# Kernel tuning notes

Hardware: AMD Instinct MI355X
Metric: run time of the kernel (lower is better)

## Reference

```python
import jax, jax.numpy as jnp
import numpy as np

D_MODEL = 128
DEPTH = 4
LN_EPS = 1e-5


def _ssm(x, Wi, A, Wo):
    # x: [B, L, D]; Wi: [3D, D]; A: [D]; Wo: [D, D]
    z = jnp.einsum('bld,ed->ble', x, Wi)          # [B, L, 3D]
    u, i, o = jnp.split(z, 3, axis=-1)
    iu = jax.nn.sigmoid(i) * jnp.tanh(u)          # gated input, [B, L, D]
    og = jax.nn.sigmoid(o)                        # output gate
    a = jnp.minimum(jnp.exp(A), 0.999)            # decay, [D]

    def step(s, c):
        s = a * s + c
        return s, s

    s0 = jnp.zeros((x.shape[0], x.shape[2]), x.dtype)
    _, S = jax.lax.scan(step, s0, jnp.swapaxes(iu, 0, 1))  # [L, B, D]
    y = og * jnp.swapaxes(S, 0, 1)                # [B, L, D]
    return jnp.einsum('bld,ed->ble', y, Wo)


def _scan_2d(x, Wi, A, Wo):
    # x: [N, D, H, W] -> four directional 1D scans, averaged
    N, D, H, W = x.shape
    xh = jnp.transpose(x, (0, 2, 3, 1))           # [N, H, W, D]
    lr = _ssm(xh.reshape(N * H, W, D), Wi, A, Wo).reshape(N, H, W, D)
    rl = _ssm(jnp.flip(xh, 2).reshape(N * H, W, D), Wi, A, Wo).reshape(N, H, W, D)
    rl = jnp.flip(rl, 2)
    xw = jnp.transpose(x, (0, 3, 2, 1))           # [N, W, H, D]
    ud = _ssm(xw.reshape(N * W, H, D), Wi, A, Wo).reshape(N, W, H, D)
    du = _ssm(jnp.flip(xw, 2).reshape(N * W, H, D), Wi, A, Wo).reshape(N, W, H, D)
    du = jnp.flip(du, 2)
    y = (lr + rl + jnp.transpose(ud, (0, 2, 1, 3)) + jnp.transpose(du, (0, 2, 1, 3))) / 4
    return jnp.transpose(y, (0, 3, 1, 2))         # [N, D, H, W]


def setup_inputs() -> dict:
    key = jax.random.key(0)
    ks = jax.random.split(key, 8)
    D = D_MODEL
    lin = 1.0 / np.sqrt(D)
    tok = jax.random.normal(ks[0], (8, 16, D, 32, 32), jnp.float32)
    s_inp = jax.random.normal(ks[1], (DEPTH, 3 * D, D), jnp.float32) * lin
    s_A = jax.random.normal(ks[2], (DEPTH, D), jnp.float32) * -0.1
    s_out = jax.random.normal(ks[3], (DEPTH, D, D), jnp.float32) * lin
    t_inp = jax.random.normal(ks[4], (DEPTH, 3 * D, D), jnp.float32) * lin
    t_A = jax.random.normal(ks[5], (DEPTH, D), jnp.float32) * -0.1
    t_out = jax.random.normal(ks[6], (DEPTH, D, D), jnp.float32) * lin
    ln_g = jnp.ones((D,), jnp.float32)
    ln_b = jnp.zeros((D,), jnp.float32)
    return {"tok": tok, "s_inp": s_inp, "s_A": s_A, "s_out": s_out,
            "t_inp": t_inp, "t_A": t_A, "t_out": t_out,
            "ln_g": ln_g, "ln_b": ln_b}


def reference(tok, s_inp, s_A, s_out, t_inp, t_A, t_out, ln_g, ln_b):
    B, T, D, h, w = tok.shape
    x = tok
    for l in range(DEPTH):
        xs = x.reshape(B * T, D, h, w)
        xs = _scan_2d(xs, s_inp[l], s_A[l], s_out[l]).reshape(B, T, D, h, w)
        xt = jnp.transpose(xs, (0, 3, 4, 1, 2)).reshape(B * h * w, T, D)
        xt = _ssm(xt, t_inp[l], t_A[l], t_out[l]).reshape(B, h, w, T, D)
        x = x + jnp.transpose(xt, (0, 3, 4, 1, 2))
    xn = jnp.transpose(x, (0, 1, 3, 4, 2))        # [B,T,h,w,D]
    mu = jnp.mean(xn, axis=-1, keepdims=True)
    var = jnp.var(xn, axis=-1, keepdims=True)
    xn = (xn - mu) / jnp.sqrt(var + LN_EPS) * ln_g + ln_b
    return jnp.transpose(xn, (0, 1, 4, 2, 3))     # [B,T,D,h,w]
```

## Files before the change

### kernel.cpp

```cpp
#include <hip/hip_runtime.h>
#include <hip/hip_bf16.h>
#include <math.h>

#define D_MODEL 128
#define HW      1024
#define DEPTH   4
#define NIMG    128
#define B_      8
#define T_      16
#define LN_EPSF 1e-5f

typedef short  s8  __attribute__((ext_vector_type(8)));
typedef ushort us8 __attribute__((ext_vector_type(8)));
typedef ushort us4 __attribute__((ext_vector_type(4)));
typedef float  f4  __attribute__((ext_vector_type(4)));

__device__ __forceinline__ float sig_(float x) { return 1.0f / (1.0f + __expf(-x)); }
__device__ __forceinline__ float tanh_(float x) { return 2.0f * sig_(2.0f * x) - 1.0f; }
__device__ __forceinline__ ushort f2b(float f) {
    __hip_bfloat16 h = __float2bfloat16(f);
    return *reinterpret_cast<ushort*>(&h);
}
__device__ __forceinline__ float b2f(ushort u) {
    __hip_bfloat16 h = *reinterpret_cast<__hip_bfloat16*>(&u);
    return __bfloat162float(h);
}

__global__ __launch_bounds__(256) void wconv_kernel(
    const float* __restrict__ src, ushort* __restrict__ dst, int n)
{
    int i = blockIdx.x * 256 + threadIdx.x;
    if (i < n) dst[i] = f2b(src[i]);
}

__device__ __forceinline__ void gates_from_lds(
    const ushort (*Xs)[136], const ushort* __restrict__ Wi,
    ushort* __restrict__ iu, ushort* __restrict__ og,
    size_t nbase, int q0, int tid)
{
    const int lane = tid & 63;
    const int wv   = tid >> 6;
    const int grp  = lane >> 4;
    const int lrow = lane & 15;
    const int ch0  = wv * 32;

    f4 aU[2][4], aI[2][4], aO[2][4];
    #pragma unroll
    for (int nt = 0; nt < 2; ++nt)
        #pragma unroll
        for (int qt = 0; qt < 4; ++qt) { aU[nt][qt] = (f4)0.f; aI[nt][qt] = (f4)0.f; aO[nt][qt] = (f4)0.f; }

    #pragma unroll
    for (int kk = 0; kk < 4; ++kk) {
        const int kb = kk * 32 + grp * 8;
        s8 xb[4], wu[2], wi[2], wo[2];
        #pragma unroll
        for (int qt = 0; qt < 4; ++qt)
            xb[qt] = *reinterpret_cast<const s8*>(&Xs[qt * 16 + lrow][kb]);
        #pragma unroll
        for (int nt = 0; nt < 2; ++nt) {
            const int e = ch0 + nt * 16 + lrow;
            wu[nt] = *reinterpret_cast<const s8*>(Wi + (size_t)e * D_MODEL + kb);
            wi[nt] = *reinterpret_cast<const s8*>(Wi + (size_t)(e + 128) * D_MODEL + kb);
            wo[nt] = *reinterpret_cast<const s8*>(Wi + (size_t)(e + 256) * D_MODEL + kb);
        }
        #pragma unroll
        for (int nt = 0; nt < 2; ++nt)
            #pragma unroll
            for (int qt = 0; qt < 4; ++qt) {
                aU[nt][qt] = __builtin_amdgcn_mfma_f32_16x16x32_bf16(wu[nt], xb[qt], aU[nt][qt], 0, 0, 0);
                aI[nt][qt] = __builtin_amdgcn_mfma_f32_16x16x32_bf16(wi[nt], xb[qt], aI[nt][qt], 0, 0, 0);
                aO[nt][qt] = __builtin_amdgcn_mfma_f32_16x16x32_bf16(wo[nt], xb[qt], aO[nt][qt], 0, 0, 0);
            }
    }

    #pragma unroll
    for (int nt = 0; nt < 2; ++nt)
        #pragma unroll
        for (int qt = 0; qt < 4; ++qt) {
            const int q = q0 + qt * 16 + lrow;
            const size_t off = nbase + (size_t)q * D_MODEL + ch0 + nt * 16 + grp * 4;
            us4 piu, pog;
            #pragma unroll
            for (int i = 0; i < 4; ++i) {
                piu[i] = f2b(sig_(aI[nt][qt][i]) * tanh_(aU[nt][qt][i]));
                pog[i] = f2b(sig_(aO[nt][qt][i]));
            }
            *reinterpret_cast<us4*>(iu + off) = piu;
            *reinterpret_cast<us4*>(og + off) = pog;
        }
}

__device__ __forceinline__ void stage1_gfrags(
    const ushort* __restrict__ S, const ushort* __restrict__ og,
    float scale, size_t nbase, int q0, int wv, int grp, int lrow, s8 g[4])
{
    const size_t rbase = nbase + (size_t)(q0 + wv * 16 + lrow) * D_MODEL + grp * 8;
    #pragma unroll
    for (int kk = 0; kk < 4; ++kk) {
        const size_t off = rbase + kk * 32;
        us8 sv = *reinterpret_cast<const us8*>(S + off);
        us8 ov = *reinterpret_cast<const us8*>(og + off);
        s8 gg;
        #pragma unroll
        for (int j = 0; j < 8; ++j)
            gg[j] = (short)f2b(b2f(sv[j]) * b2f(ov[j]) * scale);
        g[kk] = gg;
    }
}

__global__ __launch_bounds__(256, 2) void gates_f32_kernel(
    const float* __restrict__ in, const ushort* __restrict__ Wi,
    ushort* __restrict__ iu, ushort* __restrict__ og)
{
    __shared__ ushort Xs[64][136];
    const int n   = blockIdx.x >> 4;
    const int q0  = (blockIdx.x & 15) << 6;
    const int tid = threadIdx.x;
    const size_t nbase = (size_t)n * (D_MODEL * HW);

    {
        const float* inb = in + nbase + q0;
        const int q   = tid & 63;
        const int dh0 = tid >> 6;
        for (int it = 0; it < 4; ++it) {
            const int dh = dh0 + it * 4;
            s8 pk;
            #pragma unroll
            for (int j = 0; j < 8; ++j)
                pk[j] = (short)f2b(inb[(size_t)(dh * 8 + j) * HW + q]);
            *reinterpret_cast<s8*>(&Xs[q][dh * 8]) = pk;
        }
    }
    __syncthreads();
    gates_from_lds(Xs, Wi, iu, og, nbase, q0, tid);
}

__global__ __launch_bounds__(256, 2) void fusedA_kernel(
    const ushort* __restrict__ S, const ushort* __restrict__ og_in,
    const ushort* __restrict__ Wo, const ushort* __restrict__ Wi2,
    ushort* __restrict__ iu, ushort* __restrict__ og, float scale)
{
    __shared__ ushort Xs[64][136];
    const int n   = blockIdx.x >> 4;
    const int q0  = (blockIdx.x & 15) << 6;
    const int tid = threadIdx.x;
    const int lane = tid & 63, wv = tid >> 6, grp = lane >> 4, lrow = lane & 15;
    const size_t nbase = (size_t)n * (D_MODEL * HW);

    s8 g[4];
    stage1_gfrags(S, og_in, scale, nbase, q0, wv, grp, lrow, g);

    f4 C[8];
    #pragma unroll
    for (int et = 0; et < 8; ++et) C[et] = (f4)0.f;
    #pragma unroll
    for (int kk = 0; kk < 4; ++kk) {
        const int kb = kk * 32 + grp * 8;
        #pragma unroll
        for (int et = 0; et < 8; ++et) {
            s8 wf = *reinterpret_cast<const s8*>(Wo + (size_t)(et * 16 + lrow) * D_MODEL + kb);
            C[et] = __builtin_amdgcn_mfma_f32_16x16x32_bf16(g[kk], wf, C[et], 0, 0, 0);
        }
    }

    #pragma unroll
    for (int et = 0; et < 8; ++et)
        #pragma unroll
        for (int i = 0; i < 4; ++i)
            Xs[wv * 16 + grp * 4 + i][et * 16 + lrow] = f2b(C[et][i]);
    __syncthreads();

    gates_from_lds(Xs, Wi2, iu, og, nbase, q0, tid);
}

template <bool GATES, bool LN>
__global__ __launch_bounds__(256, 2) void fusedB_kernel(
    const ushort* __restrict__ S, const ushort* __restrict__ og_in,
    const ushort* __restrict__ Wo, const float* __restrict__ resid,
    float* __restrict__ X, const ushort* __restrict__ Wi2,
    ushort* __restrict__ iu, ushort* __restrict__ og,
    const float* __restrict__ lng, const float* __restrict__ lnb)
{
    __shared__ ushort Xs[64][136];
    const int n   = blockIdx.x >> 4;
    const int q0  = (blockIdx.x & 15) << 6;
    const int tid = threadIdx.x;
    const int lane = tid & 63, wv = tid >> 6, grp = lane >> 4, lrow = lane & 15;
    const size_t nbase = (size_t)n * (D_MODEL * HW);

    s8 g[4];
    stage1_gfrags(S, og_in, 1.0f, nbase, q0, wv, grp, lrow, g);

    f4 C[8];
    #pragma unroll
    for (int et = 0; et < 8; ++et) C[et] = (f4)0.f;
    #pragma unroll
    for (int kk = 0; kk < 4; ++kk) {
        const int kb = kk * 32 + grp * 8;
        #pragma unroll
        for (int et = 0; et < 8; ++et) {
            s8 wf = *reinterpret_cast<const s8*>(Wo + (size_t)(et * 16 + lrow) * D_MODEL + kb);
            C[et] = __builtin_amdgcn_mfma_f32_16x16x32_bf16(g[kk], wf, C[et], 0, 0, 0);
        }
    }

    const int qb = q0 + wv * 16 + grp * 4;

    if constexpr (LN) {
        float sum[4] = {0.f, 0.f, 0.f, 0.f}, sq[4] = {0.f, 0.f, 0.f, 0.f};
        #pragma unroll
        for (int et = 0; et < 8; ++et) {
            const int e = et * 16 + lrow;
            const size_t off = nbase + (size_t)e * HW + qb;
            f4 r = *reinterpret_cast<const f4*>(resid + off);
            #pragma unroll
            for (int i = 0; i < 4; ++i) {
                float v = C[et][i] + r[i];
                C[et][i] = v;
                sum[i] += v; sq[i] += v * v;
            }
        }
        #pragma unroll
        for (int m = 1; m <= 8; m <<= 1)
            #pragma unroll
            for (int i = 0; i < 4; ++i) {
                sum[i] += __shfl_xor(sum[i], m);
                sq[i]  += __shfl_xor(sq[i], m);
            }
        float mean[4], rstd[4];
        #pragma unroll
        for (int i = 0; i < 4; ++i) {
            mean[i] = sum[i] * (1.f / D_MODEL);
            float var = sq[i] * (1.f / D_MODEL) - mean[i] * mean[i];
            rstd[i] = rsqrtf(var + LN_EPSF);
        }
        #pragma unroll
        for (int et = 0; et < 8; ++et) {
            const int e = et * 16 + lrow;
            const float ge = lng[e], be = lnb[e];
            const size_t off = nbase + (size_t)e * HW + qb;
            f4 o;
            #pragma unroll
            for (int i = 0; i < 4; ++i)
                o[i] = (C[et][i] - mean[i]) * rstd[i] * ge + be;
            *reinterpret_cast<f4*>(X + off) = o;
        }
    } else {
        #pragma unroll
        for (int et = 0; et < 8; ++et) {
            const int e = et * 16 + lrow;
            const size_t off = nbase + (size_t)e * HW + qb;
            f4 r = *reinterpret_cast<const f4*>(resid + off);
            f4 v;
            #pragma unroll
            for (int i = 0; i < 4; ++i) v[i] = C[et][i] + r[i];
            *reinterpret_cast<f4*>(X + off) = v;
            if constexpr (GATES) {
                #pragma unroll
                for (int i = 0; i < 4; ++i)
                    Xs[wv * 16 + grp * 4 + i][e] = f2b(v[i]);
            }
        }
        if constexpr (GATES) {
            __syncthreads();
            gates_from_lds(Xs, Wi2, iu, og, nbase, q0, tid);
        }
    }
}

__global__ __launch_bounds__(256) void rowscan_kernel(
    const ushort* __restrict__ iu, ushort* __restrict__ R,
    const float* __restrict__ Av)
{
    const int tid = blockIdx.x * 256 + threadIdx.x;
    const int d = tid & 127;
    const int i = (tid >> 7) & 31;
    const int n = tid >> 12;
    const float a = fminf(__expf(Av[d]), 0.999f);
    const size_t base = (size_t)n * (D_MODEL * HW) + (size_t)(i * 32) * D_MODEL + d;

    float x[32], acc[32];
    #pragma unroll
    for (int j = 0; j < 32; ++j) x[j] = b2f(iu[base + (size_t)j * D_MODEL]);
    float s = 0.f;
    #pragma unroll
    for (int j = 0; j < 32; ++j) { s = fmaf(a, s, x[j]); acc[j] = s; }
    s = 0.f;
    #pragma unroll
    for (int j = 31; j >= 0; --j) { s = fmaf(a, s, x[j]); acc[j] += s; }
    #pragma unroll
    for (int j = 0; j < 32; ++j) R[base + (size_t)j * D_MODEL] = f2b(acc[j]);
}

__global__ __launch_bounds__(256) void colscan_kernel(
    ushort* __restrict__ buf, const ushort* __restrict__ R,
    const float* __restrict__ Av)
{
    const int tid = blockIdx.x * 256 + threadIdx.x;
    const int d = tid & 127;
    const int j = (tid >> 7) & 31;
    const int n = tid >> 12;
    const float a = fminf(__expf(Av[d]), 0.999f);
    const size_t base = (size_t)n * (D_MODEL * HW) + (size_t)j * D_MODEL + d;
    const size_t istr = (size_t)32 * D_MODEL;

    float x[32], t[32];
    #pragma unroll
    for (int i = 0; i < 32; ++i) x[i] = b2f(buf[base + i * istr]);
    float s = 0.f;
    #pragma unroll
    for (int i = 0; i < 32; ++i) { s = fmaf(a, s, x[i]); t[i] = s; }
    s = 0.f;
    #pragma unroll
    for (int i = 31; i >= 0; --i) { s = fmaf(a, s, x[i]); t[i] += s; }
    #pragma unroll
    for (int i = 0; i < 32; ++i)
        buf[base + i * istr] = f2b(t[i] + b2f(R[base + i * istr]));
}

__global__ __launch_bounds__(256) void tscan_kernel(
    ushort* __restrict__ buf, const float* __restrict__ Av)
{
    const int tid = blockIdx.x * 256 + threadIdx.x;
    const int dc = tid & 15;
    const int q  = (tid >> 4) & 1023;
    const int b  = tid >> 14;
    float aa[8], st[8];
    #pragma unroll
    for (int jj = 0; jj < 8; ++jj) {
        aa[jj] = fminf(__expf(Av[dc * 8 + jj]), 0.999f);
        st[jj] = 0.f;
    }
    #pragma unroll
    for (int t = 0; t < T_; ++t) {
        const size_t off = ((size_t)(b * T_ + t) * HW + q) * D_MODEL + dc * 8;
        us8 v = *reinterpret_cast<us8*>(buf + off);
        us8 w;
        #pragma unroll
        for (int jj = 0; jj < 8; ++jj) {
            st[jj] = fmaf(aa[jj], st[jj], b2f(v[jj]));
            w[jj] = f2b(st[jj]);
        }
        *reinterpret_cast<us8*>(buf + off) = w;
    }
}

extern "C" void kernel_launch(void* const* d_in, const int* in_sizes, int n_in,
                              void* d_out, int out_size, void* d_ws, size_t ws_size,
                              hipStream_t stream) {
    const float* tok   = (const float*)d_in[0];
    const float* s_inp = (const float*)d_in[1];
    const float* s_A   = (const float*)d_in[2];
    const float* s_out = (const float*)d_in[3];
    const float* t_inp = (const float*)d_in[4];
    const float* t_A   = (const float*)d_in[5];
    const float* t_out = (const float*)d_in[6];
    const float* ln_g  = (const float*)d_in[7];
    const float* ln_b  = (const float*)d_in[8];

    float*  X    = (float*)d_out;
    ushort* Abuf = (ushort*)d_ws;
    ushort* Bbuf = Abuf + (size_t)16777216;
    ushort* Cbuf = Bbuf + (size_t)16777216;
    ushort* Wbf  = Cbuf + (size_t)16777216;
    ushort* sWiB = Wbf;
    ushort* sWoB = Wbf + 196608;
    ushort* tWiB = Wbf + 262144;
    ushort* tWoB = Wbf + 458752;

    const dim3 blk256(256);

    wconv_kernel<<<768, blk256, 0, stream>>>(s_inp, sWiB, 196608);
    wconv_kernel<<<256, blk256, 0, stream>>>(s_out, sWoB, 65536);
    wconv_kernel<<<768, blk256, 0, stream>>>(t_inp, tWiB, 196608);
    wconv_kernel<<<256, blk256, 0, stream>>>(t_out, tWoB, 65536);

    gates_f32_kernel<<<2048, blk256, 0, stream>>>(tok, sWiB, Abuf, Bbuf);

    for (int l = 0; l < DEPTH; ++l) {
        const float* xin = (l == 0) ? tok : X;

        rowscan_kernel<<<2048, blk256, 0, stream>>>(Abuf, Cbuf, s_A + (size_t)l * 128);
        colscan_kernel<<<2048, blk256, 0, stream>>>(Abuf, Cbuf, s_A + (size_t)l * 128);
        fusedA_kernel<<<2048, blk256, 0, stream>>>(
            Abuf, Bbuf, sWoB + (size_t)l * 16384, tWiB + (size_t)l * 49152,
            Abuf, Bbuf, 0.25f);
        tscan_kernel<<<512, blk256, 0, stream>>>(Abuf, t_A + (size_t)l * 128);

        if (l < DEPTH - 1) {
            fusedB_kernel<true, false><<<2048, blk256, 0, stream>>>(
                Abuf, Bbuf, tWoB + (size_t)l * 16384, xin, X,
                sWiB + (size_t)(l + 1) * 49152, Abuf, Bbuf, nullptr, nullptr);
        } else {
            fusedB_kernel<false, true><<<2048, blk256, 0, stream>>>(
                Abuf, Bbuf, tWoB + (size_t)l * 16384, xin, X,
                nullptr, nullptr, nullptr, ln_g, ln_b);
        }
    }
}
```

Before: 850.8 us.

## Fuse row and column scans into one LDS kernel with channel-octet layout

Changes the intermediate bf16 buffers from [pixel][channel] to [channel-octet][pixel][8], so each channel group of an image becomes a contiguous 16 KB slab. The separate rowscan and colscan kernels become one scan2d kernel. It loads an octet slab into swizzled, padded LDS, runs all four directional scans there, and applies the output gate and the 1/4 average before writing back. This removes the Cbuf round-trip and the strided global accesses of the column scan, and moves the gate multiply out of fusedA. In exchange it uses about 66 KB of LDS per block, which may limit occupancy.

```diff
diff --git a/kernel.cpp b/kernel.cpp
--- a/kernel.cpp
+++ b/kernel.cpp
@@ -9,11 +9,15 @@
 #define B_      8
 #define T_      16
 #define LN_EPSF 1e-5f
+#define TLN     131072
+#define PS      1033
 
 typedef short  s8  __attribute__((ext_vector_type(8)));
 typedef ushort us8 __attribute__((ext_vector_type(8)));
 typedef ushort us4 __attribute__((ext_vector_type(4)));
 typedef float  f4  __attribute__((ext_vector_type(4)));
+
+#define MFMA __builtin_amdgcn_mfma_f32_16x16x32_bf16
 
 __device__ __forceinline__ float sig_(float x) { return 1.0f / (1.0f + __expf(-x)); }
 __device__ __forceinline__ float tanh_(float x) { return 2.0f * sig_(2.0f * x) - 1.0f; }
@@ -33,16 +37,13 @@
     if (i < n) dst[i] = f2b(src[i]);
 }
 
-__device__ __forceinline__ void gates_from_lds(
+__device__ __forceinline__ void gates_from_lds_TL(
     const ushort (*Xs)[136], const ushort* __restrict__ Wi,
     ushort* __restrict__ iu, ushort* __restrict__ og,
     size_t nbase, int q0, int tid)
 {
-    const int lane = tid & 63;
-    const int wv   = tid >> 6;
-    const int grp  = lane >> 4;
-    const int lrow = lane & 15;
-    const int ch0  = wv * 32;
+    const int lane = tid & 63, wv = tid >> 6, grp = lane >> 4, lrow = lane & 15;
+    const int ch0 = wv * 32;
 
     f4 aU[2][4], aI[2][4], aO[2][4];
     #pragma unroll
@@ -68,9 +69,9 @@
         for (int nt = 0; nt < 2; ++nt)
             #pragma unroll
             for (int qt = 0; qt < 4; ++qt) {
-                aU[nt][qt] = __builtin_amdgcn_mfma_f32_16x16x32_bf16(wu[nt], xb[qt], aU[nt][qt], 0, 0, 0);
-                aI[nt][qt] = __builtin_amdgcn_mfma_f32_16x16x32_bf16(wi[nt], xb[qt], aI[nt][qt], 0, 0, 0);
-                aO[nt][qt] = __builtin_amdgcn_mfma_f32_16x16x32_bf16(wo[nt], xb[qt], aO[nt][qt], 0, 0, 0);
+                aU[nt][qt] = MFMA(wu[nt], xb[qt], aU[nt][qt], 0, 0, 0);
+                aI[nt][qt] = MFMA(wi[nt], xb[qt], aI[nt][qt], 0, 0, 0);
+                aO[nt][qt] = MFMA(wo[nt], xb[qt], aO[nt][qt], 0, 0, 0);
             }
     }
 
@@ -78,8 +79,9 @@
     for (int nt = 0; nt < 2; ++nt)
         #pragma unroll
         for (int qt = 0; qt < 4; ++qt) {
-            const int q = q0 + qt * 16 + lrow;
-            const size_t off = nbase + (size_t)q * D_MODEL + ch0 + nt * 16 + grp * 4;
+            const int ch = ch0 + nt * 16 + grp * 4;
+            const int q  = q0 + qt * 16 + lrow;
+            const size_t off = nbase + (size_t)(ch >> 3) * 8192 + (size_t)q * 8 + (ch & 7);
             us4 piu, pog;
             #pragma unroll
             for (int i = 0; i < 4; ++i) {
@@ -91,24 +93,6 @@
         }
 }
 
-__device__ __forceinline__ void stage1_gfrags(
-    const ushort* __restrict__ S, const ushort* __restrict__ og,
-    float scale, size_t nbase, int q0, int wv, int grp, int lrow, s8 g[4])
-{
-    const size_t rbase = nbase + (size_t)(q0 + wv * 16 + lrow) * D_MODEL + grp * 8;
-    #pragma unroll
-    for (int kk = 0; kk < 4; ++kk) {
-        const size_t off = rbase + kk * 32;
-        us8 sv = *reinterpret_cast<const us8*>(S + off);
-        us8 ov = *reinterpret_cast<const us8*>(og + off);
-        s8 gg;
-        #pragma unroll
-        for (int j = 0; j < 8; ++j)
-            gg[j] = (short)f2b(b2f(sv[j]) * b2f(ov[j]) * scale);
-        g[kk] = gg;
-    }
-}
-
 __global__ __launch_bounds__(256, 2) void gates_f32_kernel(
     const float* __restrict__ in, const ushort* __restrict__ Wi,
     ushort* __restrict__ iu, ushort* __restrict__ og)
@@ -117,12 +101,11 @@
     const int n   = blockIdx.x >> 4;
     const int q0  = (blockIdx.x & 15) << 6;
     const int tid = threadIdx.x;
-    const size_t nbase = (size_t)n * (D_MODEL * HW);
+    const size_t nbase = (size_t)n * TLN;
 
     {
         const float* inb = in + nbase + q0;
-        const int q   = tid & 63;
-        const int dh0 = tid >> 6;
+        const int q = tid & 63, dh0 = tid >> 6;
         for (int it = 0; it < 4; ++it) {
             const int dh = dh0 + it * 4;
             s8 pk;
@@ -133,23 +116,99 @@
         }
     }
     __syncthreads();
-    gates_from_lds(Xs, Wi, iu, og, nbase, q0, tid);
+    gates_from_lds_TL(Xs, Wi, iu, og, nbase, q0, tid);
+}
+
+__global__ __launch_bounds__(256, 2) void scan2d_kernel(
+    ushort* bufG , const ushort* __restrict__ og,
+    const float* __restrict__ Av)
+{
+    __shared__ float P[8 * PS];
+    __shared__ float R[8 * PS];
+    const int n   = blockIdx.x >> 4;
+    const int oct = blockIdx.x & 15;
+    const int tid = threadIdx.x;
+    const size_t base = (size_t)n * TLN + (size_t)oct * 8192;
+
+    for (int it = 0; it < 4; ++it) {
+        const int p  = it * 256 + tid;
+        const int sw = p ^ (((p >> 5) & 7) << 2);
+        us8 v = *reinterpret_cast<const us8*>(bufG + base + (size_t)p * 8);
+        #pragma unroll
+        for (int dc = 0; dc < 8; ++dc) P[dc * PS + sw] = b2f(v[dc]);
+    }
+    __syncthreads();
+
+    const int dc  = tid & 7;
+    const int row = tid >> 3;
+    const float a = fminf(__expf(Av[oct * 8 + dc]), 0.999f);
+
+    {
+        const int swb = (row * 32) ^ (((row & 7) << 2));
+        float x[32], r[32];
+        #pragma unroll
+        for (int j = 0; j < 32; ++j) x[j] = P[dc * PS + (swb ^ j)];
+        float s = 0.f;
+        #pragma unroll
+        for (int j = 0; j < 32; ++j) { s = fmaf(a, s, x[j]); r[j] = s; }
+        s = 0.f;
+        #pragma unroll
+        for (int j = 31; j >= 0; --j) { s = fmaf(a, s, x[j]); r[j] += s; }
+        #pragma unroll
+        for (int j = 0; j < 32; ++j) R[dc * PS + (swb ^ j)] = r[j];
+    }
+    __syncthreads();
+
+    {
+        float x[32], t[32];
+        #pragma unroll
+        for (int i = 0; i < 32; ++i) {
+            const int p = i * 32 + row;
+            x[i] = P[dc * PS + (p ^ ((i & 7) << 2))];
+        }
+        float s = 0.f;
+        #pragma unroll
+        for (int i = 0; i < 32; ++i) { s = fmaf(a, s, x[i]); t[i] = s; }
+        s = 0.f;
+        #pragma unroll
+        for (int i = 31; i >= 0; --i) { s = fmaf(a, s, x[i]); t[i] += s; }
+        #pragma unroll
+        for (int i = 0; i < 32; ++i) {
+            const int idx = dc * PS + ((i * 32 + row) ^ ((i & 7) << 2));
+            P[idx] = t[i] + R[idx];
+        }
+    }
+    __syncthreads();
+
+    for (int it = 0; it < 4; ++it) {
+        const int p  = it * 256 + tid;
+        const int sw = p ^ (((p >> 5) & 7) << 2);
+        us8 o = *reinterpret_cast<const us8*>(og + base + (size_t)p * 8);
+        us8 w;
+        #pragma unroll
+        for (int d2 = 0; d2 < 8; ++d2)
+            w[d2] = f2b(b2f(o[d2]) * P[d2 * PS + sw] * 0.25f);
+        *reinterpret_cast<us8*>(bufG + base + (size_t)p * 8) = w;
+    }
 }
 
 __global__ __launch_bounds__(256, 2) void fusedA_kernel(
-    const ushort* __restrict__ S, const ushort* __restrict__ og_in,
-    const ushort* __restrict__ Wo, const ushort* __restrict__ Wi2,
-    ushort* __restrict__ iu, ushort* __restrict__ og, float scale)
+    ushort* bufA , ushort* bufB ,
+    const ushort* __restrict__ WoS, const ushort* __restrict__ WiT)
 {
     __shared__ ushort Xs[64][136];
     const int n   = blockIdx.x >> 4;
     const int q0  = (blockIdx.x & 15) << 6;
     const int tid = threadIdx.x;
     const int lane = tid & 63, wv = tid >> 6, grp = lane >> 4, lrow = lane & 15;
-    const size_t nbase = (size_t)n * (D_MODEL * HW);
-
-    s8 g[4];
-    stage1_gfrags(S, og_in, scale, nbase, q0, wv, grp, lrow, g);
+    const size_t nbase = (size_t)n * TLN;
+    const int qq = q0 + wv * 16 + lrow;
+
+    s8 gf[4];
+    #pragma unroll
+    for (int kk = 0; kk < 4; ++kk)
+        gf[kk] = *reinterpret_cast<const s8*>(
+            bufA + nbase + (size_t)(kk * 4 + grp) * 8192 + (size_t)qq * 8);
 
     f4 C[8];
     #pragma unroll
@@ -159,8 +218,8 @@
         const int kb = kk * 32 + grp * 8;
         #pragma unroll
         for (int et = 0; et < 8; ++et) {
-            s8 wf = *reinterpret_cast<const s8*>(Wo + (size_t)(et * 16 + lrow) * D_MODEL + kb);
-            C[et] = __builtin_amdgcn_mfma_f32_16x16x32_bf16(g[kk], wf, C[et], 0, 0, 0);
+            s8 wf = *reinterpret_cast<const s8*>(WoS + (size_t)(et * 16 + lrow) * D_MODEL + kb);
+            C[et] = MFMA(gf[kk], wf, C[et], 0, 0, 0);
         }
     }
 
@@ -171,15 +230,42 @@
             Xs[wv * 16 + grp * 4 + i][et * 16 + lrow] = f2b(C[et][i]);
     __syncthreads();
 
-    gates_from_lds(Xs, Wi2, iu, og, nbase, q0, tid);
+    gates_from_lds_TL(Xs, WiT, bufA, bufB, nbase, q0, tid);
+}
+
+__global__ __launch_bounds__(256) void tscan_kernel(
+    ushort* __restrict__ buf, const float* __restrict__ Av)
+{
+    const int tid = blockIdx.x * 256 + threadIdx.x;
+    const int q   = tid & 1023;
+    const int oct = (tid >> 10) & 15;
+    const int b   = tid >> 14;
+    float aa[8], st[8];
+    #pragma unroll
+    for (int jj = 0; jj < 8; ++jj) {
+        aa[jj] = fminf(__expf(Av[oct * 8 + jj]), 0.999f);
+        st[jj] = 0.f;
+    }
+    const size_t base = (size_t)(b * T_) * TLN + (size_t)oct * 8192 + (size_t)q * 8;
+    #pragma unroll
+    for (int t = 0; t < T_; ++t) {
+        ushort* p = buf + base + (size_t)t * TLN;
+        us8 v = *reinterpret_cast<us8*>(p);
+        us8 w;
+        #pragma unroll
+        for (int jj = 0; jj < 8; ++jj) {
+            st[jj] = fmaf(aa[jj], st[jj], b2f(v[jj]));
+            w[jj] = f2b(st[jj]);
+        }
+        *reinterpret_cast<us8*>(p) = w;
+    }
 }
 
 template <bool GATES, bool LN>
 __global__ __launch_bounds__(256, 2) void fusedB_kernel(
-    const ushort* __restrict__ S, const ushort* __restrict__ og_in,
-    const ushort* __restrict__ Wo, const float* __restrict__ resid,
-    float* __restrict__ X, const ushort* __restrict__ Wi2,
-    ushort* __restrict__ iu, ushort* __restrict__ og,
+    ushort* bufA , ushort* bufB ,
+    const ushort* __restrict__ WoT, const float* __restrict__ resid,
+    float* __restrict__ X, const ushort* __restrict__ WiS2,
     const float* __restrict__ lng, const float* __restrict__ lnb)
 {
     __shared__ ushort Xs[64][136];
@@ -187,10 +273,21 @@
     const int q0  = (blockIdx.x & 15) << 6;
     const int tid = threadIdx.x;
     const int lane = tid & 63, wv = tid >> 6, grp = lane >> 4, lrow = lane & 15;
-    const size_t nbase = (size_t)n * (D_MODEL * HW);
+    const size_t nbase = (size_t)n * TLN;
+    const int qq = q0 + wv * 16 + lrow;
 
     s8 g[4];
-    stage1_gfrags(S, og_in, 1.0f, nbase, q0, wv, grp, lrow, g);
+    #pragma unroll
+    for (int kk = 0; kk < 4; ++kk) {
+        const size_t off = nbase + (size_t)(kk * 4 + grp) * 8192 + (size_t)qq * 8;
+        us8 sv = *reinterpret_cast<const us8*>(bufA + off);
+        us8 ov = *reinterpret_cast<const us8*>(bufB + off);
+        s8 gg;
+        #pragma unroll
+        for (int j = 0; j < 8; ++j)
+            gg[j] = (short)f2b(b2f(sv[j]) * b2f(ov[j]));
+        g[kk] = gg;
+    }
 
     f4 C[8];
     #pragma unroll
@@ -200,62 +297,63 @@
         const int kb = kk * 32 + grp * 8;
         #pragma unroll
         for (int et = 0; et < 8; ++et) {
-            s8 wf = *reinterpret_cast<const s8*>(Wo + (size_t)(et * 16 + lrow) * D_MODEL + kb);
-            C[et] = __builtin_amdgcn_mfma_f32_16x16x32_bf16(g[kk], wf, C[et], 0, 0, 0);
+            s8 wf = *reinterpret_cast<const s8*>(WoT + (size_t)(et * 16 + lrow) * D_MODEL + kb);
+            C[et] = MFMA(g[kk], wf, C[et], 0, 0, 0);
         }
     }
 
     const int qb = q0 + wv * 16 + grp * 4;
+    #pragma unroll
+    for (int et = 0; et < 8; ++et) {
+        const int e = et * 16 + lrow;
+        const size_t offX = nbase + (size_t)e * HW + qb;
+        f4 r = *reinterpret_cast<const f4*>(resid + offX);
+        #pragma unroll
+        for (int i = 0; i < 4; ++i) C[et][i] += r[i];
+    }
 
     if constexpr (LN) {
-        float sum[4] = {0.f, 0.f, 0.f, 0.f}, sq[4] = {0.f, 0.f, 0.f, 0.f};
-        #pragma unroll
-        for (int et = 0; et < 8; ++et) {
-            const int e = et * 16 + lrow;
-            const size_t off = nbase + (size_t)e * HW + qb;
-            f4 r = *reinterpret_cast<const f4*>(resid + off);
+        float s4[4] = {0.f,0.f,0.f,0.f}, q4[4] = {0.f,0.f,0.f,0.f};
+        #pragma unroll
+        for (int et = 0; et < 8; ++et)
             #pragma unroll
             for (int i = 0; i < 4; ++i) {
-                float v = C[et][i] + r[i];
-                C[et][i] = v;
-                sum[i] += v; sq[i] += v * v;
+                s4[i] += C[et][i];
+                q4[i] += C[et][i] * C[et][i];
             }
-        }
         #pragma unroll
         for (int m = 1; m <= 8; m <<= 1)
             #pragma unroll
             for (int i = 0; i < 4; ++i) {
-                sum[i] += __shfl_xor(sum[i], m);
-                sq[i]  += __shfl_xor(sq[i], m);
+                s4[i] += __shfl_xor(s4[i], m);
+                q4[i] += __shfl_xor(q4[i], m);
             }
         float mean[4], rstd[4];
         #pragma unroll
         for (int i = 0; i < 4; ++i) {
-            mean[i] = sum[i] * (1.f / D_MODEL);
-            float var = sq[i] * (1.f / D_MODEL) - mean[i] * mean[i];
-            rstd[i] = rsqrtf(var + LN_EPSF);
+            mean[i] = s4[i] * (1.f / D_MODEL);
+            rstd[i] = rsqrtf(q4[i] * (1.f / D_MODEL) - mean[i] * mean[i] + LN_EPSF);
         }
         #pragma unroll
         for (int et = 0; et < 8; ++et) {
             const int e = et * 16 + lrow;
             const float ge = lng[e], be = lnb[e];
-            const size_t off = nbase + (size_t)e * HW + qb;
+            const size_t offX = nbase + (size_t)e * HW + qb;
             f4 o;
             #pragma unroll
             for (int i = 0; i < 4; ++i)
                 o[i] = (C[et][i] - mean[i]) * rstd[i] * ge + be;
-            *reinterpret_cast<f4*>(X + off) = o;
+            *reinterpret_cast<f4*>(X + offX) = o;
         }
     } else {
         #pragma unroll
         for (int et = 0; et < 8; ++et) {
             const int e = et * 16 + lrow;
-            const size_t off = nbase + (size_t)e * HW + qb;
-            f4 r = *reinterpret_cast<const f4*>(resid + off);
+            const size_t offX = nbase + (size_t)e * HW + qb;
             f4 v;
             #pragma unroll
-            for (int i = 0; i < 4; ++i) v[i] = C[et][i] + r[i];
-            *reinterpret_cast<f4*>(X + off) = v;
+            for (int i = 0; i < 4; ++i) v[i] = C[et][i];
+            *reinterpret_cast<f4*>(X + offX) = v;
             if constexpr (GATES) {
                 #pragma unroll
                 for (int i = 0; i < 4; ++i)
@@ -264,85 +362,8 @@
         }
         if constexpr (GATES) {
             __syncthreads();
-            gates_from_lds(Xs, Wi2, iu, og, nbase, q0, tid);
-        }
-    }
-}
-
-__global__ __launch_bounds__(256) void rowscan_kernel(
-    const ushort* __restrict__ iu, ushort* __restrict__ R,
-    const float* __restrict__ Av)
-{
-    const int tid = blockIdx.x * 256 + threadIdx.x;
-    const int d = tid & 127;
-    const int i = (tid >> 7) & 31;
-    const int n = tid >> 12;
-    const float a = fminf(__expf(Av[d]), 0.999f);
-    const size_t base = (size_t)n * (D_MODEL * HW) + (size_t)(i * 32) * D_MODEL + d;
-
-    float x[32], acc[32];
-    #pragma unroll
-    for (int j = 0; j < 32; ++j) x[j] = b2f(iu[base + (size_t)j * D_MODEL]);
-    float s = 0.f;
-    #pragma unroll
-    for (int j = 0; j < 32; ++j) { s = fmaf(a, s, x[j]); acc[j] = s; }
-    s = 0.f;
-    #pragma unroll
-    for (int j = 31; j >= 0; --j) { s = fmaf(a, s, x[j]); acc[j] += s; }
-    #pragma unroll
-    for (int j = 0; j < 32; ++j) R[base + (size_t)j * D_MODEL] = f2b(acc[j]);
-}
-
-__global__ __launch_bounds__(256) void colscan_kernel(
-    ushort* __restrict__ buf, const ushort* __restrict__ R,
-    const float* __restrict__ Av)
-{
-    const int tid = blockIdx.x * 256 + threadIdx.x;
-    const int d = tid & 127;
-    const int j = (tid >> 7) & 31;
-    const int n = tid >> 12;
-    const float a = fminf(__expf(Av[d]), 0.999f);
-    const size_t base = (size_t)n * (D_MODEL * HW) + (size_t)j * D_MODEL + d;
-    const size_t istr = (size_t)32 * D_MODEL;
-
-    float x[32], t[32];
-    #pragma unroll
-    for (int i = 0; i < 32; ++i) x[i] = b2f(buf[base + i * istr]);
-    float s = 0.f;
-    #pragma unroll
-    for (int i = 0; i < 32; ++i) { s = fmaf(a, s, x[i]); t[i] = s; }
-    s = 0.f;
-    #pragma unroll
-    for (int i = 31; i >= 0; --i) { s = fmaf(a, s, x[i]); t[i] += s; }
-    #pragma unroll
-    for (int i = 0; i < 32; ++i)
-        buf[base + i * istr] = f2b(t[i] + b2f(R[base + i * istr]));
-}
-
-__global__ __launch_bounds__(256) void tscan_kernel(
-    ushort* __restrict__ buf, const float* __restrict__ Av)
-{
-    const int tid = blockIdx.x * 256 + threadIdx.x;
-    const int dc = tid & 15;
-    const int q  = (tid >> 4) & 1023;
-    const int b  = tid >> 14;
-    float aa[8], st[8];
-    #pragma unroll
-    for (int jj = 0; jj < 8; ++jj) {
-        aa[jj] = fminf(__expf(Av[dc * 8 + jj]), 0.999f);
-        st[jj] = 0.f;
-    }
-    #pragma unroll
-    for (int t = 0; t < T_; ++t) {
-        const size_t off = ((size_t)(b * T_ + t) * HW + q) * D_MODEL + dc * 8;
-        us8 v = *reinterpret_cast<us8*>(buf + off);
-        us8 w;
-        #pragma unroll
-        for (int jj = 0; jj < 8; ++jj) {
-            st[jj] = fmaf(aa[jj], st[jj], b2f(v[jj]));
-            w[jj] = f2b(st[jj]);
-        }
-        *reinterpret_cast<us8*>(buf + off) = w;
+            gates_from_lds_TL(Xs, WiS2, bufA, bufB, nbase, q0, tid);
+        }
     }
 }
 
@@ -362,8 +383,7 @@
     float*  X    = (float*)d_out;
     ushort* Abuf = (ushort*)d_ws;
     ushort* Bbuf = Abuf + (size_t)16777216;
-    ushort* Cbuf = Bbuf + (size_t)16777216;
-    ushort* Wbf  = Cbuf + (size_t)16777216;
+    ushort* Wbf  = Bbuf + (size_t)16777216;
     ushort* sWiB = Wbf;
     ushort* sWoB = Wbf + 196608;
     ushort* tWiB = Wbf + 262144;
@@ -381,21 +401,19 @@
     for (int l = 0; l < DEPTH; ++l) {
         const float* xin = (l == 0) ? tok : X;
 
-        rowscan_kernel<<<2048, blk256, 0, stream>>>(Abuf, Cbuf, s_A + (size_t)l * 128);
-        colscan_kernel<<<2048, blk256, 0, stream>>>(Abuf, Cbuf, s_A + (size_t)l * 128);
+        scan2d_kernel<<<2048, blk256, 0, stream>>>(Abuf, Bbuf, s_A + (size_t)l * 128);
         fusedA_kernel<<<2048, blk256, 0, stream>>>(
-            Abuf, Bbuf, sWoB + (size_t)l * 16384, tWiB + (size_t)l * 49152,
-            Abuf, Bbuf, 0.25f);
+            Abuf, Bbuf, sWoB + (size_t)l * 16384, tWiB + (size_t)l * 49152);
         tscan_kernel<<<512, blk256, 0, stream>>>(Abuf, t_A + (size_t)l * 128);
 
         if (l < DEPTH - 1) {
             fusedB_kernel<true, false><<<2048, blk256, 0, stream>>>(
                 Abuf, Bbuf, tWoB + (size_t)l * 16384, xin, X,
-                sWiB + (size_t)(l + 1) * 49152, Abuf, Bbuf, nullptr, nullptr);
+                sWiB + (size_t)(l + 1) * 49152, nullptr, nullptr);
         } else {
             fusedB_kernel<false, true><<<2048, blk256, 0, stream>>>(
                 Abuf, Bbuf, tWoB + (size_t)l * 16384, xin, X,
-                nullptr, nullptr, nullptr, ln_g, ln_b);
-        }
-    }
-}
+                nullptr, ln_g, ln_b);
+        }
+    }
+}
```

After: 749.5 us. -11.9%, faster.
